# Kernel optimization log

Hardware: AMD Instinct MI355X
Metric: run time of the kernel (lower is better)

## Reference

```python
import jax, jax.numpy as jnp
import numpy as np

B, S, D = 1, 8192, 1024
H, HD = 16, 64
WIN = 1024      # sliding_window_size
CHUNK = 1024    # chunk_size
OVERLAP = 128   # chunk_overlap


def setup_inputs() -> dict:
    key = jax.random.key(0)
    ks = jax.random.split(key, 5)
    s = 1.0 / np.sqrt(D)
    inp = {"x": jax.random.normal(ks[0], (B, S, D), jnp.float32)}
    for i, n in enumerate(["Wq", "Wk", "Wv", "Wo"]):
        inp[n] = jax.random.normal(ks[1 + i], (D, D), jnp.float32) * s
    for n in ["bq", "bk", "bv", "bo"]:
        inp[n] = jnp.zeros((D,), jnp.float32)
    return inp


def _attend_chunk(q, k, v, chunk_start, win_start):
    # q: [B, Lq, H, HD]; k, v: [B, Lk, H, HD]
    Lq, Lk = q.shape[1], k.shape[1]
    q_abs = chunk_start + jnp.arange(Lq)[:, None]   # absolute query positions
    k_abs = win_start + jnp.arange(Lk)[None, :]     # absolute key positions
    allowed = (k_abs >= q_abs - WIN // 2) & (k_abs < q_abs + WIN // 2)
    scale = 1.0 / np.sqrt(HD)
    scores = jnp.einsum('bqhd,bkhd->bhqk', q, k) * scale  # [B,H,Lq,Lk]
    scores = jnp.where(allowed[None, None], scores, -jnp.inf)
    p = jax.nn.softmax(scores, axis=-1)
    return jnp.einsum('bhqk,bkhd->bqhd', p, v)


def _overlap_weight(cs, ce):
    # replicate torch linspace overlap-add blend weights (host-side constants)
    w = np.ones(ce - cs, np.float32)
    if cs > 0:
        n = min(cs + OVERLAP, ce) - cs
        w[:n] = np.linspace(0.0, 1.0, n, dtype=np.float32)
    if ce < S:
        os_ = max(cs, ce - OVERLAP)
        w[os_ - cs:] = np.linspace(1.0, 0.0, ce - os_, dtype=np.float32)
    return jnp.asarray(w)


def reference(x, Wq, bq, Wk, bk, Wv, bv, Wo, bo):
    q = (x @ Wq.T + bq).reshape(B, S, H, HD)
    k = (x @ Wk.T + bk).reshape(B, S, H, HD)
    v = (x @ Wv.T + bv).reshape(B, S, H, HD)
    out = jnp.zeros((B, S, H, HD), x.dtype)
    step = CHUNK - OVERLAP
    for cs in range(0, S, step):  # static Python loop over ~10 chunks
        ce = min(cs + CHUNK, S)
        ws, we = max(0, cs - WIN // 2), min(S, ce + WIN // 2)
        o = _attend_chunk(q[:, cs:ce], k[:, ws:we], v[:, ws:we], cs, ws)
        w = _overlap_weight(cs, ce)
        out = out.at[:, cs:ce].add(o * w[None, :, None, None])
    out = out.reshape(B, S, D)
    return out @ Wo.T + bo
```

## Files before the change

### kernel.cpp

```cpp
#include <hip/hip_runtime.h>

#define DEVI __device__ __forceinline__

constexpr int S = 8192, D = 1024, H = 16, HD = 64;
constexpr int NQKV = 3 * D;

typedef __attribute__((ext_vector_type(8))) __bf16 bf16x8;
typedef __attribute__((ext_vector_type(4))) __bf16 bf16x4;
typedef __attribute__((ext_vector_type(8))) unsigned short us8;
typedef __attribute__((ext_vector_type(4))) float f32x4;

DEVI unsigned short f2b(float f) {
  unsigned int u = __float_as_uint(f);
  u += 0x7fff + ((u >> 16) & 1);
  return (unsigned short)(u >> 16);
}

DEVI ushort4 cvt4(float4 v) {
  ushort4 r; r.x = f2b(v.x); r.y = f2b(v.y); r.z = f2b(v.z); r.w = f2b(v.w); return r;
}

DEVI void load_lds16b(const void* g, void* l) {
  __builtin_amdgcn_global_load_lds((const __attribute__((address_space(1))) void*)g,
                                   (__attribute__((address_space(3))) void*)l,
                                   16, 0, 0);
}

__global__ void prep_kernel(const float4* __restrict__ x,
                            const float4* __restrict__ Wq, const float4* __restrict__ Wk,
                            const float4* __restrict__ Wv, const float4* __restrict__ Wo,
                            const float4* __restrict__ bq, const float4* __restrict__ bk,
                            const float4* __restrict__ bv,
                            ushort4* __restrict__ xb, ushort4* __restrict__ wqkv,
                            ushort4* __restrict__ wob, float4* __restrict__ biasq)
{
  constexpr int NX = S * D / 4;
  constexpr int NW = D * D / 4;
  constexpr int NB = D / 4;
  constexpr int TOT = NX + 4 * NW + 3 * NB;
  for (int i = blockIdx.x * blockDim.x + threadIdx.x; i < TOT; i += gridDim.x * blockDim.x) {
    if (i < NX) {
      xb[i] = cvt4(x[i]);
    } else if (i < NX + 3 * NW) {
      int j = i - NX;
      const float4* src = (j < NW) ? Wq : ((j < 2 * NW) ? Wk : Wv);
      int jj = (j < NW) ? j : ((j < 2 * NW) ? j - NW : j - 2 * NW);
      wqkv[j] = cvt4(src[jj]);
    } else if (i < NX + 4 * NW) {
      int j = i - NX - 3 * NW;
      wob[j] = cvt4(Wo[j]);
    } else {
      int j = i - NX - 4 * NW;
      const float4* src = (j < NB) ? bq : ((j < 2 * NB) ? bk : bv);
      int jj = (j < NB) ? j : ((j < 2 * NB) ? j - NB : j - 2 * NB);
      biasq[j] = src[jj];
    }
  }
}

template<int LDC, bool OUT_BF16>
__global__ __launch_bounds__(256)
void gemm_nt(const unsigned short* __restrict__ A,
             const unsigned short* __restrict__ B,
             const float* __restrict__ bias,
             void* __restrict__ C, int K)
{
  __shared__ __align__(16) unsigned short As[128 * 32];
  __shared__ __align__(16) unsigned short Bs[128 * 32];
  const int tid = threadIdx.x;
  const int wave = tid >> 6, lane = tid & 63;
  const int quad = lane >> 4, l15 = lane & 15;
  const int m0 = blockIdx.x * 128, n0 = blockIdx.y * 128;
  const int wr = wave >> 1, wc = wave & 1;

  const f32x4 fzero = {0.f, 0.f, 0.f, 0.f};
  f32x4 acc[4][4];
#pragma unroll
  for (int i = 0; i < 4; ++i)
#pragma unroll
    for (int j = 0; j < 4; ++j) acc[i][j] = fzero;

  const int segr = lane >> 2;
  const int cpst = lane & 3;

  for (int k0 = 0; k0 < K; k0 += 32) {
    __syncthreads();
#pragma unroll
    for (int j = 0; j < 4; ++j) {
      const int s = wave * 4 + j;
      const int s7 = s & 7;
      const int r = s7 * 16 + segr;
      const int c = cpst ^ ((r >> 1) & 3);
      const unsigned short* g = (s < 8)
        ? A + (size_t)(m0 + r) * K + k0 + c * 8
        : B + (size_t)(n0 + r) * K + k0 + c * 8;
      unsigned short* l = ((s < 8) ? As : Bs) + s7 * 512;
      load_lds16b(g, l);
    }
    __syncthreads();

    bf16x8 af[4], bfr[4];
#pragma unroll
    for (int it = 0; it < 4; ++it) {
      const int r = wr * 64 + it * 16 + l15;
      const int cp = quad ^ ((r >> 1) & 3);
      af[it] = *(const bf16x8*)&As[r * 32 + cp * 8];
    }
#pragma unroll
    for (int jt = 0; jt < 4; ++jt) {
      const int r = wc * 64 + jt * 16 + l15;
      const int cp = quad ^ ((r >> 1) & 3);
      bfr[jt] = *(const bf16x8*)&Bs[r * 32 + cp * 8];
    }
#pragma unroll
    for (int it = 0; it < 4; ++it)
#pragma unroll
      for (int jt = 0; jt < 4; ++jt)
        acc[it][jt] = __builtin_amdgcn_mfma_f32_16x16x32_bf16(af[it], bfr[jt], acc[it][jt], 0, 0, 0);
  }

#pragma unroll
  for (int it = 0; it < 4; ++it)
#pragma unroll
    for (int jt = 0; jt < 4; ++jt) {
      const int col = n0 + wc * 64 + jt * 16 + l15;
      const float bv = bias[col];
#pragma unroll
      for (int i = 0; i < 4; ++i) {
        const int row = m0 + wr * 64 + it * 16 + quad * 4 + i;
        const float v = acc[it][jt][i] + bv;
        if constexpr (OUT_BF16)
          ((unsigned short*)C)[(size_t)row * LDC + col] = f2b(v);
        else
          ((float*)C)[(size_t)row * LDC + col] = v;
      }
    }
}

__global__ __launch_bounds__(256)
void transpose_v(const unsigned short* __restrict__ qkv, unsigned short* __restrict__ vtb)
{
  __shared__ unsigned short T[64 * 72];
  const int tid = threadIdx.x;
  const int kb = blockIdx.x, h = blockIdx.y;
  const unsigned short* Vp = qkv + 2 * D + h * HD;
  const int key = tid >> 3, sg = tid & 7;
#pragma unroll
  for (int r = 0; r < 2; ++r) {
    us8 v = *(const us8*)(Vp + (size_t)(kb * 64 + key + r * 32) * NQKV + sg * 8);
    unsigned short* dst = &T[sg * 8 * 72 + key + r * 32];
#pragma unroll
    for (int j = 0; j < 8; ++j) dst[j * 72] = v[j];
  }
  __syncthreads();
  const int d = tid >> 2, kc = tid & 3;
  us8* outp = (us8*)(vtb + (size_t)h * HD * S + (size_t)d * S + kb * 64 + kc * 16);
  outp[0] = *(const us8*)&T[d * 72 + kc * 16];
  outp[1] = *(const us8*)&T[d * 72 + kc * 16 + 8];
}

__global__ __launch_bounds__(256)
void attn_fused(const unsigned short* __restrict__ qkv,
                const unsigned short* __restrict__ vtb,
                unsigned short* __restrict__ attnb)
{
  __shared__ __align__(16) unsigned short Ks[2][64 * 64];
  __shared__ __align__(16) unsigned short Vt[2][64 * 64];
  __shared__ __align__(16) unsigned short Ps[4][2][16 * 72];
  const int tid = threadIdx.x;
  const int wave = tid >> 6, lane = tid & 63;
  const int quad = lane >> 4, l15 = lane & 15;
  const int h = blockIdx.y;
  const int q0 = blockIdx.x * 128;
  const int wq0 = q0 + wave * 32;

  const unsigned short* Qp = qkv + h * HD;
  const unsigned short* Kp = qkv + D + h * HD;
  const unsigned short* Vh = vtb + (size_t)h * HD * S;

  bf16x8 qf[2][2];
#pragma unroll
  for (int rt = 0; rt < 2; ++rt)
#pragma unroll
    for (int ksp = 0; ksp < 2; ++ksp)
      qf[rt][ksp] = *(const bf16x8*)(Qp + (size_t)(wq0 + rt * 16 + l15) * NQKV + ksp * 32 + quad * 8);

  const f32x4 fzero = {0.f, 0.f, 0.f, 0.f};
  f32x4 o[2][4];
  float lr[2] = {0.f, 0.f};
#pragma unroll
  for (int rt = 0; rt < 2; ++rt)
#pragma unroll
    for (int vt2 = 0; vt2 < 4; ++vt2) o[rt][vt2] = fzero;

  const int ks = (q0 >= 512) ? (q0 - 512) : 0;
  const int ke = (q0 + 640 < S) ? (q0 + 640) : S;

  const int srow = tid >> 3;
  const int sg   = tid & 7;
  const int scol = sg ^ (srow & 7);

#define STAGE(kt_, b_)                                                            \
  {                                                                               \
    _Pragma("unroll")                                                             \
    for (int r = 0; r < 2; ++r) {                                                 \
      load_lds16b(Kp + (size_t)((kt_) + srow + r * 32) * NQKV + scol * 8,         \
                  &Ks[b_][(size_t)tid * 8 + r * 2048]);                           \
      load_lds16b(Vh + (size_t)(srow + r * 32) * S + (kt_) + scol * 8,            \
                  &Vt[b_][(size_t)tid * 8 + r * 2048]);                           \
    }                                                                             \
  }

  STAGE(ks, 0);

  constexpr float L2E8 = 0.18033688011112042f;

  int b = 0;
  for (int kt = ks; kt < ke; kt += 64, b ^= 1) {
    __syncthreads();
    if (kt + 64 < ke) STAGE(kt + 64, b ^ 1);

    if (kt + 63 >= wq0 - 512 && kt <= wq0 + 542) {
      bf16x8 kf[4][2];
#pragma unroll
      for (int hh = 0; hh < 4; ++hh)
#pragma unroll
        for (int ksp = 0; ksp < 2; ++ksp)
          kf[hh][ksp] = *(const bf16x8*)&Ks[b][(hh * 16 + l15) * 64
                                              + ((ksp * 4 + quad) ^ (l15 & 7)) * 8];

#pragma unroll
      for (int st = 0; st < 2; ++st) {
        const int C0 = kt + st * 32;
#pragma unroll
        for (int rt = 0; rt < 2; ++rt) {
          const int R = wq0 + rt * 16;
          if (!((C0 + 31 >= R - 512) && (C0 <= R + 526))) continue;
          const int qa = R + l15;
          unsigned short* Pw = (unsigned short*)Ps[wave][rt];
#pragma unroll
          for (int hh2 = 0; hh2 < 2; ++hh2) {
            const int hh = st * 2 + hh2;
            const int C = C0 + hh2 * 16;
            const bool any  = (C + 15 >= R - 512) && (C <= R + 526);
            const bool full = (C >= R - 497) && (C <= R + 496);
            float p[4];
            if (!any) {
              p[0] = p[1] = p[2] = p[3] = 0.f;
            } else {
              f32x4 z0 = fzero, z1 = fzero;
              z0 = __builtin_amdgcn_mfma_f32_16x16x32_bf16(kf[hh][0], qf[rt][0], z0, 0, 0, 0);
              z1 = __builtin_amdgcn_mfma_f32_16x16x32_bf16(kf[hh][1], qf[rt][1], z1, 0, 0, 0);
              const f32x4 z = z0 + z1;
              if (full) {
#pragma unroll
                for (int i = 0; i < 4; ++i) p[i] = __builtin_amdgcn_exp2f(z[i] * L2E8);
              } else {
                const int base = C + quad * 4 - qa + 512;
#pragma unroll
                for (int i = 0; i < 4; ++i)
                  p[i] = ((unsigned)(base + i) < 1024u) ? __builtin_amdgcn_exp2f(z[i] * L2E8) : 0.f;
              }
            }
            lr[rt] += p[0] + p[1] + p[2] + p[3];
            f32x4 pv = {p[0], p[1], p[2], p[3]};
            *(bf16x4*)&Pw[l15 * 72 + hh * 16 + quad * 4] = __builtin_convertvector(pv, bf16x4);
          }
        }
      }

#pragma unroll
      for (int st = 0; st < 2; ++st) {
        const int C0 = kt + st * 32;
        if (!((C0 + 31 >= wq0 - 512) && (C0 <= wq0 + 542))) continue;
        bf16x8 vf[4];
#pragma unroll
        for (int vt2 = 0; vt2 < 4; ++vt2) {
          const int d = vt2 * 16 + l15;
          vf[vt2] = *(const bf16x8*)&Vt[b][d * 64 + (((st * 4 + quad) ^ (d & 7))) * 8];
        }
#pragma unroll
        for (int rt = 0; rt < 2; ++rt) {
          const int R = wq0 + rt * 16;
          if (!((C0 + 31 >= R - 512) && (C0 <= R + 526))) continue;
          const bf16x8 pf = *(const bf16x8*)&Ps[wave][rt][l15 * 72 + (st * 4 + quad) * 8];
#pragma unroll
          for (int vt2 = 0; vt2 < 4; ++vt2)
            o[rt][vt2] = __builtin_amdgcn_mfma_f32_16x16x32_bf16(pf, vf[vt2], o[rt][vt2], 0, 0, 0);
        }
      }
    }
  }

  float lt[2];
#pragma unroll
  for (int rt = 0; rt < 2; ++rt) {
    float l = lr[rt];
    l += __shfl_xor(l, 16);
    l += __shfl_xor(l, 32);
    lt[rt] = l;
  }
#pragma unroll
  for (int rt = 0; rt < 2; ++rt)
#pragma unroll
    for (int i = 0; i < 4; ++i) {
      const float lq = __shfl(lt[rt], quad * 4 + i);
      const int qa = wq0 + rt * 16 + quad * 4 + i;
      const float w = (qa >= S - 128) ? (1.0f + (float)(qa - (S - 128)) * (1.0f / 127.0f)) : 1.0f;
      const float scl = w / lq;
#pragma unroll
      for (int vt2 = 0; vt2 < 4; ++vt2)
        ((__bf16*)attnb)[(size_t)qa * D + h * HD + vt2 * 16 + l15] = (__bf16)(o[rt][vt2][i] * scl);
    }
#undef STAGE
}

extern "C" void kernel_launch(void* const* d_in, const int* in_sizes, int n_in,
                              void* d_out, int out_size, void* d_ws, size_t ws_size,
                              hipStream_t stream)
{
  const float* x  = (const float*)d_in[0];
  const float* Wq = (const float*)d_in[1];
  const float* Wk = (const float*)d_in[2];
  const float* Wv = (const float*)d_in[3];
  const float* Wo = (const float*)d_in[4];
  const float* bq = (const float*)d_in[5];
  const float* bk = (const float*)d_in[6];
  const float* bv = (const float*)d_in[7];
  const float* bo = (const float*)d_in[8];

  char* ws = (char*)d_ws;
  unsigned short* xb    = (unsigned short*)(ws);
  unsigned short* wqkv  = (unsigned short*)(ws + 16777216);
  unsigned short* wob   = (unsigned short*)(ws + 23068672);
  float*          biasq = (float*)         (ws + 25165824);
  unsigned short* qkv   = (unsigned short*)(ws + 25178112);
  unsigned short* attnb = (unsigned short*)(ws + 75509760);
  unsigned short* vtb   = xb;

  prep_kernel<<<2048, 256, 0, stream>>>((const float4*)x, (const float4*)Wq, (const float4*)Wk,
                                        (const float4*)Wv, (const float4*)Wo, (const float4*)bq,
                                        (const float4*)bk, (const float4*)bv,
                                        (ushort4*)xb, (ushort4*)wqkv, (ushort4*)wob, (float4*)biasq);

  gemm_nt<NQKV, true><<<dim3(64, 24), 256, 0, stream>>>(xb, wqkv, biasq, (void*)qkv, D);
  transpose_v<<<dim3(S / 64, H), 256, 0, stream>>>(qkv, vtb);
  attn_fused<<<dim3(S / 128, H), 256, 0, stream>>>(qkv, vtb, attnb);
  gemm_nt<D, false><<<dim3(64, 8), 256, 0, stream>>>(attnb, wob, bo, d_out, D);
}
```

Measured before the change: 303.6 us.

## Use 32x32 MFMA tiles in attention, remap blocks, double-buffer GEMM LDS

The attention kernel moves from 16x16x32 to 32x32x16 bf16 MFMA, so each wave handles 32 queries against 32-key slabs. P is staged through a swizzled 32x64 LDS tile, and the row-sum is reduced with fewer shuffles. Block ids are remapped so heads interleave across consecutive blocks, which may improve cache locality. The GEMM gains double-buffered LDS with the next k-tile prefetched, dropping one barrier per iteration. The trade-off is coarser masking granularity and higher register and LDS use.

After: 274.1 us. -9.7%, faster.

```diff
diff --git a/kernel.cpp b/kernel.cpp
--- a/kernel.cpp
+++ b/kernel.cpp
@@ -9,6 +9,7 @@
 typedef __attribute__((ext_vector_type(4))) __bf16 bf16x4;
 typedef __attribute__((ext_vector_type(8))) unsigned short us8;
 typedef __attribute__((ext_vector_type(4))) float f32x4;
+typedef __attribute__((ext_vector_type(16))) float f32x16;
 
 DEVI unsigned short f2b(float f) {
   unsigned int u = __float_as_uint(f);
@@ -65,8 +66,8 @@
              const float* __restrict__ bias,
              void* __restrict__ C, int K)
 {
-  __shared__ __align__(16) unsigned short As[128 * 32];
-  __shared__ __align__(16) unsigned short Bs[128 * 32];
+  __shared__ __align__(16) unsigned short As[2][128 * 32];
+  __shared__ __align__(16) unsigned short Bs[2][128 * 32];
   const int tid = threadIdx.x;
   const int wave = tid >> 6, lane = tid & 63;
   const int quad = lane >> 4, l15 = lane & 15;
@@ -83,34 +84,40 @@
   const int segr = lane >> 2;
   const int cpst = lane & 3;
 
-  for (int k0 = 0; k0 < K; k0 += 32) {
+#define GST(k0_, b_)                                                              \
+  {                                                                               \
+    _Pragma("unroll")                                                             \
+    for (int j = 0; j < 4; ++j) {                                                 \
+      const int s = wave * 4 + j;                                                 \
+      const int s7 = s & 7;                                                       \
+      const int r = s7 * 16 + segr;                                               \
+      const int c = cpst ^ ((r >> 1) & 3);                                        \
+      const unsigned short* g = (s < 8)                                           \
+        ? A + (size_t)(m0 + r) * K + (k0_) + c * 8                                \
+        : B + (size_t)(n0 + r) * K + (k0_) + c * 8;                               \
+      unsigned short* l = ((s < 8) ? As[b_] : Bs[b_]) + s7 * 512;                 \
+      load_lds16b(g, l);                                                          \
+    }                                                                             \
+  }
+
+  GST(0, 0);
+  int b = 0;
+  for (int k0 = 0; k0 < K; k0 += 32, b ^= 1) {
     __syncthreads();
-#pragma unroll
-    for (int j = 0; j < 4; ++j) {
-      const int s = wave * 4 + j;
-      const int s7 = s & 7;
-      const int r = s7 * 16 + segr;
-      const int c = cpst ^ ((r >> 1) & 3);
-      const unsigned short* g = (s < 8)
-        ? A + (size_t)(m0 + r) * K + k0 + c * 8
-        : B + (size_t)(n0 + r) * K + k0 + c * 8;
-      unsigned short* l = ((s < 8) ? As : Bs) + s7 * 512;
-      load_lds16b(g, l);
-    }
-    __syncthreads();
+    if (k0 + 32 < K) GST(k0 + 32, b ^ 1);
 
     bf16x8 af[4], bfr[4];
 #pragma unroll
     for (int it = 0; it < 4; ++it) {
       const int r = wr * 64 + it * 16 + l15;
       const int cp = quad ^ ((r >> 1) & 3);
-      af[it] = *(const bf16x8*)&As[r * 32 + cp * 8];
+      af[it] = *(const bf16x8*)&As[b][r * 32 + cp * 8];
     }
 #pragma unroll
     for (int jt = 0; jt < 4; ++jt) {
       const int r = wc * 64 + jt * 16 + l15;
       const int cp = quad ^ ((r >> 1) & 3);
-      bfr[jt] = *(const bf16x8*)&Bs[r * 32 + cp * 8];
+      bfr[jt] = *(const bf16x8*)&Bs[b][r * 32 + cp * 8];
     }
 #pragma unroll
     for (int it = 0; it < 4; ++it)
@@ -118,6 +125,7 @@
       for (int jt = 0; jt < 4; ++jt)
         acc[it][jt] = __builtin_amdgcn_mfma_f32_16x16x32_bf16(af[it], bfr[jt], acc[it][jt], 0, 0, 0);
   }
+#undef GST
 
 #pragma unroll
   for (int it = 0; it < 4; ++it)
@@ -166,32 +174,31 @@
 {
   __shared__ __align__(16) unsigned short Ks[2][64 * 64];
   __shared__ __align__(16) unsigned short Vt[2][64 * 64];
-  __shared__ __align__(16) unsigned short Ps[4][2][16 * 72];
+  __shared__ __align__(16) unsigned short Ps[4][32 * 64];
   const int tid = threadIdx.x;
   const int wave = tid >> 6, lane = tid & 63;
-  const int quad = lane >> 4, l15 = lane & 15;
-  const int h = blockIdx.y;
-  const int q0 = blockIdx.x * 128;
+  const int l31 = lane & 31, hi = lane >> 5;
+
+  const int id = blockIdx.x + 64 * blockIdx.y;
+  const int h  = (id & 7) * 2 + ((id >> 3) >> 6);
+  const int q0 = ((id >> 3) & 63) * 128;
   const int wq0 = q0 + wave * 32;
 
   const unsigned short* Qp = qkv + h * HD;
   const unsigned short* Kp = qkv + D + h * HD;
   const unsigned short* Vh = vtb + (size_t)h * HD * S;
 
-  bf16x8 qf[2][2];
-#pragma unroll
-  for (int rt = 0; rt < 2; ++rt)
-#pragma unroll
-    for (int ksp = 0; ksp < 2; ++ksp)
-      qf[rt][ksp] = *(const bf16x8*)(Qp + (size_t)(wq0 + rt * 16 + l15) * NQKV + ksp * 32 + quad * 8);
-
-  const f32x4 fzero = {0.f, 0.f, 0.f, 0.f};
-  f32x4 o[2][4];
-  float lr[2] = {0.f, 0.f};
-#pragma unroll
-  for (int rt = 0; rt < 2; ++rt)
-#pragma unroll
-    for (int vt2 = 0; vt2 < 4; ++vt2) o[rt][vt2] = fzero;
+  bf16x8 qf[4];
+#pragma unroll
+  for (int m = 0; m < 4; ++m)
+    qf[m] = *(const bf16x8*)(Qp + (size_t)(wq0 + l31) * NQKV + m * 16 + hi * 8);
+
+  f32x16 o[2];
+#pragma unroll
+  for (int n = 0; n < 2; ++n)
+#pragma unroll
+    for (int r = 0; r < 16; ++r) o[n][r] = 0.f;
+  float lr = 0.f;
 
   const int ks = (q0 >= 512) ? (q0 - 512) : 0;
   const int ke = (q0 + 640 < S) ? (q0 + 640) : S;
@@ -220,99 +227,80 @@
     __syncthreads();
     if (kt + 64 < ke) STAGE(kt + 64, b ^ 1);
 
-    if (kt + 63 >= wq0 - 512 && kt <= wq0 + 542) {
-      bf16x8 kf[4][2];
-#pragma unroll
-      for (int hh = 0; hh < 4; ++hh)
-#pragma unroll
-        for (int ksp = 0; ksp < 2; ++ksp)
-          kf[hh][ksp] = *(const bf16x8*)&Ks[b][(hh * 16 + l15) * 64
-                                              + ((ksp * 4 + quad) ^ (l15 & 7)) * 8];
-
-#pragma unroll
-      for (int st = 0; st < 2; ++st) {
-        const int C0 = kt + st * 32;
-#pragma unroll
-        for (int rt = 0; rt < 2; ++rt) {
-          const int R = wq0 + rt * 16;
-          if (!((C0 + 31 >= R - 512) && (C0 <= R + 526))) continue;
-          const int qa = R + l15;
-          unsigned short* Pw = (unsigned short*)Ps[wave][rt];
-#pragma unroll
-          for (int hh2 = 0; hh2 < 2; ++hh2) {
-            const int hh = st * 2 + hh2;
-            const int C = C0 + hh2 * 16;
-            const bool any  = (C + 15 >= R - 512) && (C <= R + 526);
-            const bool full = (C >= R - 497) && (C <= R + 496);
-            float p[4];
-            if (!any) {
-              p[0] = p[1] = p[2] = p[3] = 0.f;
-            } else {
-              f32x4 z0 = fzero, z1 = fzero;
-              z0 = __builtin_amdgcn_mfma_f32_16x16x32_bf16(kf[hh][0], qf[rt][0], z0, 0, 0, 0);
-              z1 = __builtin_amdgcn_mfma_f32_16x16x32_bf16(kf[hh][1], qf[rt][1], z1, 0, 0, 0);
-              const f32x4 z = z0 + z1;
-              if (full) {
-#pragma unroll
-                for (int i = 0; i < 4; ++i) p[i] = __builtin_amdgcn_exp2f(z[i] * L2E8);
-              } else {
-                const int base = C + quad * 4 - qa + 512;
-#pragma unroll
-                for (int i = 0; i < 4; ++i)
-                  p[i] = ((unsigned)(base + i) < 1024u) ? __builtin_amdgcn_exp2f(z[i] * L2E8) : 0.f;
-              }
+    if (kt + 63 >= wq0 - 512 && kt <= wq0 + 31 + 511) {
+      unsigned short* Pw = (unsigned short*)Ps[wave];
+
+#pragma unroll
+      for (int kb2 = 0; kb2 < 2; ++kb2) {
+        const int C0 = kt + kb2 * 32;
+        const bool any = (C0 + 31 >= wq0 - 512) && (C0 <= wq0 + 31 + 511);
+        float p[16];
+        if (!any) {
+#pragma unroll
+          for (int r = 0; r < 16; ++r) p[r] = 0.f;
+        } else {
+          bf16x8 kf[4];
+#pragma unroll
+          for (int m = 0; m < 4; ++m)
+            kf[m] = *(const bf16x8*)&Ks[b][(kb2 * 32 + l31) * 64 + ((m * 2 + hi) ^ (l31 & 7)) * 8];
+          f32x16 z;
+#pragma unroll
+          for (int r = 0; r < 16; ++r) z[r] = 0.f;
+#pragma unroll
+          for (int m = 0; m < 4; ++m)
+            z = __builtin_amdgcn_mfma_f32_32x32x16_bf16(kf[m], qf[m], z, 0, 0, 0);
+
+          const bool full = (C0 >= wq0 - 481) && (C0 <= wq0 + 480);
+          if (full) {
+#pragma unroll
+            for (int r = 0; r < 16; ++r) p[r] = __builtin_amdgcn_exp2f(z[r] * L2E8);
+          } else {
+            const int base = C0 + 4 * hi - (wq0 + l31) + 512;
+#pragma unroll
+            for (int r = 0; r < 16; ++r) {
+              const int u = base + (r & 3) + 8 * (r >> 2);
+              p[r] = ((unsigned)u < 1024u) ? __builtin_amdgcn_exp2f(z[r] * L2E8) : 0.f;
             }
-            lr[rt] += p[0] + p[1] + p[2] + p[3];
-            f32x4 pv = {p[0], p[1], p[2], p[3]};
-            *(bf16x4*)&Pw[l15 * 72 + hh * 16 + quad * 4] = __builtin_convertvector(pv, bf16x4);
           }
         }
-      }
-
-#pragma unroll
-      for (int st = 0; st < 2; ++st) {
-        const int C0 = kt + st * 32;
-        if (!((C0 + 31 >= wq0 - 512) && (C0 <= wq0 + 542))) continue;
-        bf16x8 vf[4];
-#pragma unroll
-        for (int vt2 = 0; vt2 < 4; ++vt2) {
-          const int d = vt2 * 16 + l15;
-          vf[vt2] = *(const bf16x8*)&Vt[b][d * 64 + (((st * 4 + quad) ^ (d & 7))) * 8];
-        }
-#pragma unroll
-        for (int rt = 0; rt < 2; ++rt) {
-          const int R = wq0 + rt * 16;
-          if (!((C0 + 31 >= R - 512) && (C0 <= R + 526))) continue;
-          const bf16x8 pf = *(const bf16x8*)&Ps[wave][rt][l15 * 72 + (st * 4 + quad) * 8];
-#pragma unroll
-          for (int vt2 = 0; vt2 < 4; ++vt2)
-            o[rt][vt2] = __builtin_amdgcn_mfma_f32_16x16x32_bf16(pf, vf[vt2], o[rt][vt2], 0, 0, 0);
+#pragma unroll
+        for (int r = 0; r < 16; ++r) lr += p[r];
+#pragma unroll
+        for (int g = 0; g < 4; ++g) {
+          f32x4 pv = {p[g * 4], p[g * 4 + 1], p[g * 4 + 2], p[g * 4 + 3]};
+          const int p8 = kb2 * 4 + g;
+          *(bf16x4*)&Pw[l31 * 64 + (p8 ^ (l31 & 7)) * 8 + hi * 4] = __builtin_convertvector(pv, bf16x4);
         }
       }
-    }
-  }
-
-  float lt[2];
-#pragma unroll
-  for (int rt = 0; rt < 2; ++rt) {
-    float l = lr[rt];
-    l += __shfl_xor(l, 16);
-    l += __shfl_xor(l, 32);
-    lt[rt] = l;
-  }
-#pragma unroll
-  for (int rt = 0; rt < 2; ++rt)
-#pragma unroll
-    for (int i = 0; i < 4; ++i) {
-      const float lq = __shfl(lt[rt], quad * 4 + i);
-      const int qa = wq0 + rt * 16 + quad * 4 + i;
-      const float w = (qa >= S - 128) ? (1.0f + (float)(qa - (S - 128)) * (1.0f / 127.0f)) : 1.0f;
-      const float scl = w / lq;
-#pragma unroll
-      for (int vt2 = 0; vt2 < 4; ++vt2)
-        ((__bf16*)attnb)[(size_t)qa * D + h * HD + vt2 * 16 + l15] = (__bf16)(o[rt][vt2][i] * scl);
-    }
+
+      bf16x8 pf[4];
+#pragma unroll
+      for (int s = 0; s < 4; ++s)
+        pf[s] = *(const bf16x8*)&Pw[l31 * 64 + ((s * 2 + hi) ^ (l31 & 7)) * 8];
+#pragma unroll
+      for (int n = 0; n < 2; ++n)
+#pragma unroll
+        for (int s = 0; s < 4; ++s) {
+          const int d = n * 32 + l31;
+          const bf16x8 vf = *(const bf16x8*)&Vt[b][d * 64 + ((s * 2 + hi) ^ (l31 & 7)) * 8];
+          o[n] = __builtin_amdgcn_mfma_f32_32x32x16_bf16(pf[s], vf, o[n], 0, 0, 0);
+        }
+    }
+  }
 #undef STAGE
+
+  lr += __shfl_xor(lr, 32);
+#pragma unroll
+  for (int r = 0; r < 16; ++r) {
+    const int qr = (r & 3) + 8 * (r >> 2) + 4 * hi;
+    const float lq = __shfl(lr, qr);
+    const int qa = wq0 + qr;
+    const float w = (qa >= S - 128) ? (1.0f + (float)(qa - (S - 128)) * (1.0f / 127.0f)) : 1.0f;
+    const float scl = w / lq;
+#pragma unroll
+    for (int n = 0; n < 2; ++n)
+      ((__bf16*)attnb)[(size_t)qa * D + h * HD + n * 32 + l31] = (__bf16)(o[n][r] * scl);
+  }
 }
 
 extern "C" void kernel_launch(void* const* d_in, const int* in_sizes, int n_in,
```
